# Performance work log

Hardware: AMD Instinct MI355X
Metric: run time of the kernel (lower is better)

## Reference

```python
import jax, jax.numpy as jnp
import numpy as np

B, N, K, D = 16, 16384, 16, 256  # batch, num feature tokens, num slots, slot/feature dim
FEAT = 256
LN_EPS = 1e-5


def _ln(x, g, b):
    m = jnp.mean(x, -1, keepdims=True)
    v = jnp.mean((x - m) ** 2, -1, keepdims=True)
    return (x - m) * jax.lax.rsqrt(v + LN_EPS) * g + b


def setup_inputs() -> dict:
    key = jax.random.key(0)
    ks = jax.random.split(key, 18)
    s = 0.02
    return {
        "features": jax.random.normal(ks[0], (B, N, FEAT), jnp.float32),
        "slots_init": jax.random.normal(ks[1], (B, K, D), jnp.float32),
        "g_f": jnp.ones((FEAT,), jnp.float32), "b_f": jnp.zeros((FEAT,), jnp.float32),
        "g_s": jnp.ones((D,), jnp.float32), "b_s": jnp.zeros((D,), jnp.float32),
        "g_m": jnp.ones((D,), jnp.float32), "b_m": jnp.zeros((D,), jnp.float32),
        "Wq": jax.random.normal(ks[2], (D, D), jnp.float32) * s,
        "Wk": jax.random.normal(ks[3], (D, FEAT), jnp.float32) * s,
        "Wv": jax.random.normal(ks[4], (D, FEAT), jnp.float32) * s,
        "w_ih": jax.random.normal(ks[5], (3 * D, D), jnp.float32) * s,
        "w_hh": jax.random.normal(ks[6], (3 * D, D), jnp.float32) * s,
        "b_ih": jnp.zeros((3 * D,), jnp.float32),
        "b_hh": jnp.zeros((3 * D,), jnp.float32),
        "W1": jax.random.normal(ks[7], (4 * D, D), jnp.float32) * s,
        "b1": jnp.zeros((4 * D,), jnp.float32),
        "W2": jax.random.normal(ks[8], (D, 4 * D), jnp.float32) * s,
        "b2": jnp.zeros((D,), jnp.float32),
        "num_src_view": 4,
    }


def reference(features, slots_init, g_f, b_f, g_s, b_s, g_m, b_m, Wq, Wk, Wv,
              w_ih, w_hh, b_ih, b_hh, W1, b1, W2, b2, num_src_view):
    f = _ln(features, g_f, b_f)            # [B,N,FEAT]
    k = f @ Wk.T                            # [B,N,D]
    v = f @ Wv.T                            # [B,N,D]
    scale = float(D) ** -0.5                # num_head = 1, head-mean is identity

    def gru(x, h):  # PyTorch GRUCell math, batched over [B,K]
        gi = x @ w_ih.T + b_ih
        gh = h @ w_hh.T + b_hh
        ir, iz, inn = jnp.split(gi, 3, -1)
        hr, hz, hn = jnp.split(gh, 3, -1)
        r = jax.nn.sigmoid(ir + hr)
        z = jax.nn.sigmoid(iz + hz)
        n = jnp.tanh(inn + r * hn)
        return (1.0 - z) * n + z * h

    def one_iter(slots):
        q = _ln(slots, g_s, b_s) @ Wq.T                         # [B,K,D]
        logits = jnp.einsum('bkd,bnd->bkn', q, k) * scale       # [B,K,N]
        attn = jax.nn.softmax(logits, axis=1)                   # competitive over slots
        attn_wm = attn / (jnp.sum(attn, -1, keepdims=True) + 1.0)  # epsilon = 1.0
        updates = jnp.einsum('bkn,bnd->bkd', attn_wm, v)        # [B,K,D]
        h = gru(updates, slots)
        h = h + (jax.nn.relu(_ln(h, g_m, b_m) @ W1.T + b1) @ W2.T + b2)
        return h, attn

    slots = slots_init
    for _ in range(2):  # num_iter - 1 iterations with straight-through detach trick
        slots, _ = one_iter(slots)
        slots = jax.lax.stop_gradient(slots) + slots_init - jax.lax.stop_gradient(slots_init)
    slots, attn = one_iter(slots)
    return slots, attn
```

## Files before the change

kernel.cpp:

```cpp
#include <hip/hip_runtime.h>
#include <cstdint>
#include <cstddef>

#define BB    16
#define NTOK  16384
#define KS    16
#define DD    256
#define FEATN 256
#define NBLK  32
#define LN_EPS 1e-5f

typedef float        float4v __attribute__((ext_vector_type(4)));
typedef unsigned int uint4v  __attribute__((ext_vector_type(4)));
typedef unsigned int uint2v  __attribute__((ext_vector_type(2)));
typedef __bf16       bf16x8  __attribute__((ext_vector_type(8)));

__device__ __forceinline__ float bflo(unsigned u){ return __builtin_bit_cast(float, u << 16); }
__device__ __forceinline__ float bfhi(unsigned u){ return __builtin_bit_cast(float, u & 0xffff0000u); }
__device__ __forceinline__ unsigned short f2bf(float v){ __bf16 b = (__bf16)v; return __builtin_bit_cast(unsigned short, b); }
__device__ __forceinline__ float sigm(float x){ return 1.f/(1.f + __expf(-x)); }

__global__ void prep_w_kernel(const float* __restrict__ Wv, const float* __restrict__ w_ih,
                              const float* __restrict__ w_hh, const float* __restrict__ W1,
                              const float* __restrict__ W2, const float* __restrict__ Wq,
                              const float* __restrict__ Wk,
                              unsigned short* __restrict__ Wv_t, unsigned short* __restrict__ wih_t,
                              unsigned short* __restrict__ whh_t, unsigned short* __restrict__ W1_t,
                              unsigned short* __restrict__ W2_t, unsigned short* __restrict__ Wq_t,
                              unsigned short* __restrict__ Wk_b)
{
  __shared__ float tile[64][65];
  const int t = blockIdx.x, tid = threadIdx.x;
  const float* src; unsigned short* dst; int R, C, base;
  if      (t < 16)  { src = Wv;   dst = Wv_t;  R = 256;  C = 256;  base = 0;   }
  else if (t < 64)  { src = w_ih; dst = wih_t; R = 768;  C = 256;  base = 16;  }
  else if (t < 112) { src = w_hh; dst = whh_t; R = 768;  C = 256;  base = 64;  }
  else if (t < 176) { src = W1;   dst = W1_t;  R = 1024; C = 256;  base = 112; }
  else if (t < 240) { src = W2;   dst = W2_t;  R = 256;  C = 1024; base = 176; }
  else if (t < 256) { src = Wq;   dst = Wq_t;  R = 256;  C = 256;  base = 240; }
  else {
    const int t2 = t - 256;
    for (int i = tid; i < 4096; i += 256) {
      const int idx = t2*4096 + i;
      Wk_b[idx] = f2bf(Wk[idx]);
    }
    return;
  }
  const int tt = t - base;
  const int tiles_r = R >> 6;
  const int r0 = (tt % tiles_r) * 64, c0 = (tt / tiles_r) * 64;
  const int j = tid & 63, i0 = (tid >> 6) * 16;
  for (int s = 0; s < 16; ++s)
    tile[i0 + s][j] = src[(size_t)(r0 + i0 + s)*C + c0 + j];
  __syncthreads();
  for (int s = 0; s < 16; ++s) {
    const int i = i0 + s;
    dst[(size_t)(c0 + i)*R + r0 + j] = f2bf(tile[j][i]);
  }
}

__device__ __forceinline__ void lnqu_tail_p(
    const float* Vs, float* Ys, float* Qs, float* Pp, float* SUb, float* CBb,
    const float* __restrict__ g_s, const float* __restrict__ b_s,
    const unsigned short* __restrict__ Wq_t, const unsigned short* __restrict__ Wk_b,
    const float* __restrict__ g_f, const float* __restrict__ b_f,
    unsigned short* __restrict__ u_buf, float* __restrict__ su_buf, float* __restrict__ cb_buf,
    int b, int k0, int tid)
{
  const int w = tid >> 6, L = tid & 63;
  {
    const float v0 = Vs[w*256+L], v1 = Vs[w*256+64+L], v2 = Vs[w*256+128+L], v3 = Vs[w*256+192+L];
    float s = v0+v1+v2+v3;
    #pragma unroll
    for (int m = 1; m < 64; m <<= 1) s += __shfl_xor(s, m);
    const float mean = s * (1.f/DD);
    const float d0 = v0-mean, d1 = v1-mean, d2 = v2-mean, d3 = v3-mean;
    float s2 = d0*d0 + d1*d1 + d2*d2 + d3*d3;
    #pragma unroll
    for (int m = 1; m < 64; m <<= 1) s2 += __shfl_xor(s2, m);
    const float rs = rsqrtf(s2 * (1.f/DD) + LN_EPS);
    Ys[L*4+w]       = d0*rs*g_s[L]      + b_s[L];
    Ys[(64+L)*4+w]  = d1*rs*g_s[64+L]   + b_s[64+L];
    Ys[(128+L)*4+w] = d2*rs*g_s[128+L]  + b_s[128+L];
    Ys[(192+L)*4+w] = d3*rs*g_s[192+L]  + b_s[192+L];
  }
  __syncthreads();
  {
    float acc[4][4] = {};
    for (int cc = w*64; cc < w*64+64; ++cc) {
      const float4v xv = *reinterpret_cast<const float4v*>(Ys + cc*4);
      const uint2v wr = *reinterpret_cast<const uint2v*>(Wq_t + (size_t)cc*DD + 4*L);
      const float w0 = bflo(wr[0]), w1 = bfhi(wr[0]), w2 = bflo(wr[1]), w3 = bfhi(wr[1]);
      #pragma unroll
      for (int s = 0; s < 4; ++s) {
        acc[s][0] += xv[s]*w0; acc[s][1] += xv[s]*w1;
        acc[s][2] += xv[s]*w2; acc[s][3] += xv[s]*w3;
      }
    }
    #pragma unroll
    for (int s = 0; s < 4; ++s)
      *reinterpret_cast<float4v*>(Pp + (w*4+s)*256 + 4*L) = *reinterpret_cast<const float4v*>(acc[s]);
  }
  __syncthreads();
  for (int i = tid; i < 4*DD; i += 256) {
    const int kk = i >> 8, d = i & 255;
    Qs[d*4+kk] = Pp[(0*4+kk)*256+d] + Pp[(1*4+kk)*256+d] + Pp[(2*4+kk)*256+d] + Pp[(3*4+kk)*256+d];
  }
  __syncthreads();
  {
    float acc[4][4] = {};
    for (int d = w*64; d < w*64+64; ++d) {
      const float4v xv = *reinterpret_cast<const float4v*>(Qs + d*4);
      const uint2v wr = *reinterpret_cast<const uint2v*>(Wk_b + (size_t)d*DD + 4*L);
      const float w0 = bflo(wr[0]), w1 = bfhi(wr[0]), w2 = bflo(wr[1]), w3 = bfhi(wr[1]);
      #pragma unroll
      for (int s = 0; s < 4; ++s) {
        acc[s][0] += xv[s]*w0; acc[s][1] += xv[s]*w1;
        acc[s][2] += xv[s]*w2; acc[s][3] += xv[s]*w3;
      }
    }
    #pragma unroll
    for (int s = 0; s < 4; ++s)
      *reinterpret_cast<float4v*>(Pp + (w*4+s)*256 + 4*L) = *reinterpret_cast<const float4v*>(acc[s]);
  }
  __syncthreads();
  for (int i = tid; i < 4*DD; i += 256) {
    const int kk = i >> 8, cc = i & 255;
    const float qk = Pp[(0*4+kk)*256+cc] + Pp[(1*4+kk)*256+cc] + Pp[(2*4+kk)*256+cc] + Pp[(3*4+kk)*256+cc];
    const float uv = qk * g_f[cc];
    u_buf[(size_t)(b*KS + k0 + kk)*DD + cc] = f2bf(uv);
    SUb[kk*256+cc] = uv;
    CBb[kk*256+cc] = qk * b_f[cc];
  }
  __syncthreads();
  {
    float s  = SUb[w*256+L] + SUb[w*256+64+L] + SUb[w*256+128+L] + SUb[w*256+192+L];
    float cv = CBb[w*256+L] + CBb[w*256+64+L] + CBb[w*256+128+L] + CBb[w*256+192+L];
    #pragma unroll
    for (int m = 1; m < 64; m <<= 1) { s += __shfl_xor(s, m); cv += __shfl_xor(cv, m); }
    if (L == 0) { su_buf[b*KS + k0 + w] = s; cb_buf[b*KS + k0 + w] = cv; }
  }
}

__global__ void k0_kernel(const float* __restrict__ slots_init,
                          const float* __restrict__ g_s, const float* __restrict__ b_s,
                          const unsigned short* __restrict__ Wq_t, const unsigned short* __restrict__ Wk_b,
                          const float* __restrict__ g_f, const float* __restrict__ b_f,
                          unsigned short* __restrict__ u_buf, float* __restrict__ su_buf,
                          float* __restrict__ cb_buf)
{
  const int b = blockIdx.x >> 2, k0 = (blockIdx.x & 3) * 4;
  const int tid = threadIdx.x;
  __shared__ __align__(16) float Vs[4*DD];
  __shared__ __align__(16) float Ys[DD*4];
  __shared__ __align__(16) float Qs[DD*4];
  __shared__ __align__(16) float Pp[4*4*DD];
  __shared__ __align__(16) float SUb[4*DD];
  __shared__ __align__(16) float CBb[4*DD];
  for (int i = tid; i < 4*DD; i += 256)
    Vs[i] = slots_init[(size_t)(b*KS + k0)*DD + i];
  __syncthreads();
  lnqu_tail_p(Vs, Ys, Qs, Pp, SUb, CBb, g_s, b_s, Wq_t, Wk_b, g_f, b_f,
              u_buf, su_buf, cb_buf, b, k0, tid);
}

template<int MODE, int LAST>
__launch_bounds__(256, 1)
__global__ void phaseA_kernel(const float* __restrict__ feat,
                              unsigned short* __restrict__ xb, float* __restrict__ stats,
                              const unsigned short* __restrict__ u_buf,
                              const float* __restrict__ su_buf,
                              const float* __restrict__ cb_buf,
                              float* __restrict__ P_part,
                              float* __restrict__ S_part,
                              float* __restrict__ R_part,
                              float* __restrict__ attn_out)
{
  __shared__ __align__(16) unsigned int xl[4][128*36];
  __shared__ float ssh[4][16];
  __shared__ float rsh[4][16];

  const int b   = blockIdx.x / NBLK;
  const int blk = blockIdx.x - b*NBLK;
  const int tid = threadIdx.x;
  const int w = tid >> 6;
  const int l = tid & 63;
  const int c = l & 15;
  const int g = l >> 4;

  bf16x8 ufrag[8];
  {
    const bf16x8* up = reinterpret_cast<const bf16x8*>(u_buf + (size_t)(b*KS + c)*DD);
    #pragma unroll
    for (int kk = 0; kk < 8; ++kk) ufrag[kk] = up[4*kk + g];
  }
  const float su_c = su_buf[b*KS + c];
  const float cb_c = cb_buf[b*KS + c];

  float4v Pacc[16];
  #pragma unroll
  for (int t = 0; t < 16; ++t) Pacc[t] = (float4v){0.f,0.f,0.f,0.f};
  float S_acc = 0.f, R_acc = 0.f;

  unsigned int* myxl = xl[w];
  const int rbase = 8*(c>>2) + (c&3);

  for (int pass = 0; pass < 4; ++pass) {
    const int n0 = blk*(NTOK/NBLK) + pass*128 + w*32;
    float4v Ct[2];
    float m_t[2], rs_t[2];

    if constexpr (MODE == 1) {
      bf16x8 xr0[8], xr1[8];
      float2 st0, st1;
      {
        const size_t row0 = (size_t)b*NTOK + (size_t)(n0 + rbase);
        const size_t row1 = row0 + 4;
        const bf16x8* p0v = reinterpret_cast<const bf16x8*>(xb + row0*FEATN);
        const bf16x8* p1v = reinterpret_cast<const bf16x8*>(xb + row1*FEATN);
        #pragma unroll
        for (int kk = 0; kk < 8; ++kk) { xr0[kk] = p0v[4*kk + g]; xr1[kk] = p1v[4*kk + g]; }
        st0 = *reinterpret_cast<const float2*>(stats + row0*2);
        st1 = *reinterpret_cast<const float2*>(stats + row1*2);
      }
      #pragma unroll
      for (int tp = 0; tp < 2; ++tp) {
        const int nloc = rbase + 4*tp;
        float4v Cacc = (float4v){0.f,0.f,0.f,0.f};
        #pragma unroll
        for (int kk = 0; kk < 8; ++kk) {
          const bf16x8 af = tp ? xr1[kk] : xr0[kk];
          const uint4v ad = __builtin_bit_cast(uint4v, af);
          const int pb = (16*kk + 4*g)*36 + nloc;
          myxl[pb      ] = ad[0];
          myxl[pb + 36 ] = ad[1];
          myxl[pb + 72 ] = ad[2];
          myxl[pb + 108] = ad[3];
          Cacc = __builtin_amdgcn_mfma_f32_16x16x32_bf16(af, ufrag[kk], Cacc, 0, 0, 0);
        }
        m_t[tp]  = tp ? st1.x : st0.x;
        rs_t[tp] = tp ? st1.y : st0.y;
        Ct[tp]   = Cacc;
      }
    } else {
      #pragma unroll
      for (int tp = 0; tp < 2; ++tp) {
        const int nloc = rbase + 4*tp;
        const size_t row = (size_t)b*NTOK + (size_t)(n0 + nloc);
        const float* fr = feat + row*FEATN;
        float4v xf[16];
        #pragma unroll
        for (int kk = 0; kk < 8; ++kk) {
          xf[2*kk]   = *reinterpret_cast<const float4v*>(fr + 32*kk + 8*g);
          xf[2*kk+1] = *reinterpret_cast<const float4v*>(fr + 32*kk + 8*g + 4);
        }
        unsigned short* xw = xb + row*FEATN;
        float sum = 0.f, sq = 0.f;
        float4v Cacc = (float4v){0.f,0.f,0.f,0.f};
        #pragma unroll
        for (int kk = 0; kk < 8; ++kk) {
          const float4v x0 = xf[2*kk], x1 = xf[2*kk+1];
          sum += x0[0]+x0[1]+x0[2]+x0[3] + x1[0]+x1[1]+x1[2]+x1[3];
          sq  += x0[0]*x0[0]+x0[1]*x0[1]+x0[2]*x0[2]+x0[3]*x0[3]
               + x1[0]*x1[0]+x1[1]*x1[1]+x1[2]*x1[2]+x1[3]*x1[3];
          bf16x8 af;
          af[0]=(__bf16)x0[0]; af[1]=(__bf16)x0[1]; af[2]=(__bf16)x0[2]; af[3]=(__bf16)x0[3];
          af[4]=(__bf16)x1[0]; af[5]=(__bf16)x1[1]; af[6]=(__bf16)x1[2]; af[7]=(__bf16)x1[3];
          *reinterpret_cast<bf16x8*>(xw + 32*kk + 8*g) = af;
          const uint4v ad = __builtin_bit_cast(uint4v, af);
          const int pb = (16*kk + 4*g)*36 + nloc;
          myxl[pb      ] = ad[0];
          myxl[pb + 36 ] = ad[1];
          myxl[pb + 72 ] = ad[2];
          myxl[pb + 108] = ad[3];
          Cacc = __builtin_amdgcn_mfma_f32_16x16x32_bf16(af, ufrag[kk], Cacc, 0, 0, 0);
        }
        sum += __shfl_xor(sum,16); sum += __shfl_xor(sum,32);
        sq  += __shfl_xor(sq ,16); sq  += __shfl_xor(sq ,32);
        const float mean = sum * (1.f/FEATN);
        const float var  = sq  * (1.f/FEATN) - mean*mean;
        m_t[tp]  = mean;
        rs_t[tp] = rsqrtf(var + LN_EPS);
        float2 st; st.x = m_t[tp]; st.y = rs_t[tp];
        *reinterpret_cast<float2*>(stats + row*2) = st;
        Ct[tp] = Cacc;
      }
    }

    float arr[8];
    #pragma unroll
    for (int tp = 0; tp < 2; ++tp) {
      float lv[4], rsr[4], mr[4];
      #pragma unroll
      for (int r = 0; r < 4; ++r) {
        const int src = 4*g + r;
        rsr[r] = __shfl(rs_t[tp], src);
        mr[r]  = __shfl(m_t[tp],  src);
        lv[r]  = 0.0625f * (rsr[r]*(Ct[tp][r] - mr[r]*su_c) + cb_c);
      }
      float a_[4];
      #pragma unroll
      for (int r = 0; r < 4; ++r) {
        float v = lv[r];
        v = fmaxf(v, __shfl_xor(v,1));
        v = fmaxf(v, __shfl_xor(v,2));
        v = fmaxf(v, __shfl_xor(v,4));
        v = fmaxf(v, __shfl_xor(v,8));
        const float e = __expf(lv[r] - v);
        float s = e;
        s += __shfl_xor(s,1);
        s += __shfl_xor(s,2);
        s += __shfl_xor(s,4);
        s += __shfl_xor(s,8);
        const float a = e / s;
        a_[r] = a;
        S_acc += a;
        R_acc += a * rsr[r] * mr[r];
        arr[4*tp + r] = a * rsr[r];
      }
      if (LAST) {
        float4v av = {a_[0], a_[1], a_[2], a_[3]};
        *reinterpret_cast<float4v*>(attn_out + (size_t)(b*KS + c)*NTOK + (size_t)(n0 + 8*g + 4*tp)) = av;
      }
    }
    bf16x8 afrag;
    #pragma unroll
    for (int j = 0; j < 8; ++j) afrag[j] = (__bf16)arr[j];

    #pragma unroll
    for (int t = 0; t < 16; ++t) {
      const unsigned int* rp = &myxl[(t*8 + (c>>1))*36 + 8*g];
      const uint4v q0 = *reinterpret_cast<const uint4v*>(rp);
      const uint4v q1 = *reinterpret_cast<const uint4v*>(rp + 4);
      const unsigned int sel = (c & 1) ? 0x07060302u : 0x05040100u;
      uint4v bd;
      bd[0] = __builtin_amdgcn_perm(q0[1], q0[0], sel);
      bd[1] = __builtin_amdgcn_perm(q0[3], q0[2], sel);
      bd[2] = __builtin_amdgcn_perm(q1[1], q1[0], sel);
      bd[3] = __builtin_amdgcn_perm(q1[3], q1[2], sel);
      const bf16x8 bfrag = __builtin_bit_cast(bf16x8, bd);
      Pacc[t] = __builtin_amdgcn_mfma_f32_16x16x32_bf16(afrag, bfrag, Pacc[t], 0, 0, 0);
    }
  }

  S_acc += __shfl_xor(S_acc,16); S_acc += __shfl_xor(S_acc,32);
  R_acc += __shfl_xor(R_acc,16); R_acc += __shfl_xor(R_acc,32);
  if (g == 0) { ssh[w][c] = S_acc; rsh[w][c] = R_acc; }

  float* pf = reinterpret_cast<float*>(myxl);
  #pragma unroll
  for (int t = 0; t < 16; ++t) {
    #pragma unroll
    for (int r = 0; r < 4; ++r) pf[(4*g + r)*256 + t*16 + c] = Pacc[t][r];
  }
  __syncthreads();
  {
    float* outp = P_part + (size_t)blockIdx.x * (KS*DD);
    const float* p0 = reinterpret_cast<const float*>(&xl[0][0]);
    const float* p1 = p0 + 4608;
    const float* p2 = p0 + 9216;
    const float* p3 = p0 + 13824;
    for (int i = tid; i < KS*DD; i += 256) outp[i] = p0[i]+p1[i]+p2[i]+p3[i];
    if (tid < KS) {
      S_part[blockIdx.x*KS + tid] = ssh[0][tid]+ssh[1][tid]+ssh[2][tid]+ssh[3][tid];
      R_part[blockIdx.x*KS + tid] = rsh[0][tid]+rsh[1][tid]+rsh[2][tid]+rsh[3][tid];
    }
  }
}

template<int LAST, int NEXT>
__global__ void fusedB_kernel(const float* __restrict__ P_part, const float* __restrict__ S_part,
                              const float* __restrict__ R_part, const float* __restrict__ slots_in,
                              const float* __restrict__ g_f, const float* __restrict__ b_f,
                              const unsigned short* __restrict__ Wv_t,
                              const unsigned short* __restrict__ wih_t,
                              const unsigned short* __restrict__ whh_t,
                              const float* __restrict__ b_ih, const float* __restrict__ b_hh,
                              const float* __restrict__ g_m, const float* __restrict__ b_m,
                              const unsigned short* __restrict__ W1_t, const float* __restrict__ b1,
                              const unsigned short* __restrict__ W2_t, const float* __restrict__ b2v,
                              const float* __restrict__ g_s, const float* __restrict__ b_s,
                              const unsigned short* __restrict__ Wq_t,
                              const unsigned short* __restrict__ Wk_b,
                              float* __restrict__ slots_next, float* __restrict__ out_slots,
                              unsigned short* __restrict__ u_buf, float* __restrict__ su_buf,
                              float* __restrict__ cb_buf)
{
  const int b = blockIdx.x >> 4, k = blockIdx.x & 15;
  const int tid = threadIdx.x;
  const int w = tid >> 6, L = tid & 63;

  __shared__ __align__(16) float arena[9984];
  __shared__ float SRsh[2];
  __shared__ float redsh[8];

  float* Pp    = arena;
  float* Hsh   = arena + 6144;
  float* Tsh   = arena + 6400;
  float* Ush   = arena + 6656;
  float* Gish  = arena + 6912;
  float* Ghsh  = arena + 7680;
  float* Hpsh  = arena + 8448;
  float* Ysh   = arena + 8704;
  float* Hidsh = arena + 8960;

  Hsh[tid] = slots_in[(size_t)(b*KS + k)*DD + tid];
  if (tid < 64) {
    const int p = tid & 31;
    const float* sp = (tid < 32) ? S_part : R_part;
    float v = sp[(b*NBLK + p)*KS + k];
    v += __shfl_xor(v, 1); v += __shfl_xor(v, 2); v += __shfl_xor(v, 4);
    v += __shfl_xor(v, 8); v += __shfl_xor(v, 16);
    if (p == 0) SRsh[tid >> 5] = v;
  }
  __syncthreads();

  {
    const float S = SRsh[0], R = SRsh[1];
    const float inv = 1.f / (S + 1.f);
    const float* pb = P_part + (size_t)(b*NBLK)*KS*DD + (size_t)k*DD + tid;
    float p0 = 0.f, p1 = 0.f, p2 = 0.f, p3 = 0.f;
    #pragma unroll 2
    for (int p = 0; p < NBLK; p += 4) {
      p0 += pb[(size_t)(p+0)*KS*DD];
      p1 += pb[(size_t)(p+1)*KS*DD];
      p2 += pb[(size_t)(p+2)*KS*DD];
      p3 += pb[(size_t)(p+3)*KS*DD];
    }
    const float P = (p0 + p1) + (p2 + p3);
    Tsh[tid] = (g_f[tid]*(P - R) + S*b_f[tid]) * inv;
  }
  __syncthreads();

  {
    const int c0 = 4*L;
    float a0 = 0.f, a1 = 0.f, a2 = 0.f, a3 = 0.f;
    for (int cc = w*64; cc < w*64+64; ++cc) {
      const float x = Tsh[cc];
      const uint2v wr = *reinterpret_cast<const uint2v*>(Wv_t + (size_t)cc*DD + c0);
      a0 += x*bflo(wr[0]); a1 += x*bfhi(wr[0]);
      a2 += x*bflo(wr[1]); a3 += x*bfhi(wr[1]);
    }
    float4v av = {a0, a1, a2, a3};
    *reinterpret_cast<float4v*>(Pp + w*256 + c0) = av;
  }
  __syncthreads();
  Ush[tid] = Pp[tid] + Pp[256+tid] + Pp[512+tid] + Pp[768+tid];
  __syncthreads();

  {
    const int c0 = 4*L;
    float ai[3][4] = {}, ah[3][4] = {};
    for (int cc = w*64; cc < w*64+64; ++cc) {
      const float xi = Ush[cc], xh = Hsh[cc];
      #pragma unroll
      for (int c = 0; c < 3; ++c) {
        const uint2v wi = *reinterpret_cast<const uint2v*>(wih_t + (size_t)cc*768 + c0 + 256*c);
        const uint2v wh = *reinterpret_cast<const uint2v*>(whh_t + (size_t)cc*768 + c0 + 256*c);
        ai[c][0] += xi*bflo(wi[0]); ai[c][1] += xi*bfhi(wi[0]);
        ai[c][2] += xi*bflo(wi[1]); ai[c][3] += xi*bfhi(wi[1]);
        ah[c][0] += xh*bflo(wh[0]); ah[c][1] += xh*bfhi(wh[0]);
        ah[c][2] += xh*bflo(wh[1]); ah[c][3] += xh*bfhi(wh[1]);
      }
    }
    #pragma unroll
    for (int c = 0; c < 3; ++c) {
      *reinterpret_cast<float4v*>(Pp + w*768 + 256*c + c0)        = *reinterpret_cast<const float4v*>(ai[c]);
      *reinterpret_cast<float4v*>(Pp + 3072 + w*768 + 256*c + c0) = *reinterpret_cast<const float4v*>(ah[c]);
    }
  }
  __syncthreads();
  for (int j = tid; j < 768; j += 256) {
    Gish[j] = b_ih[j] + Pp[j] + Pp[768+j] + Pp[1536+j] + Pp[2304+j];
    Ghsh[j] = b_hh[j] + Pp[3072+j] + Pp[3840+j] + Pp[4608+j] + Pp[5376+j];
  }
  __syncthreads();

  {
    const int d = tid;
    const float r = sigm(Gish[d] + Ghsh[d]);
    const float z = sigm(Gish[256+d] + Ghsh[256+d]);
    const float n = tanhf(Gish[512+d] + r*Ghsh[512+d]);
    const float hp = (1.f - z)*n + z*Hsh[d];
    Hpsh[d] = hp;
    float s = hp;
    #pragma unroll
    for (int m = 1; m < 64; m <<= 1) s += __shfl_xor(s, m);
    if (L == 0) redsh[w] = s;
    __syncthreads();
    const float mean = (redsh[0]+redsh[1]+redsh[2]+redsh[3]) * (1.f/DD);
    const float dv = hp - mean;
    float s2 = dv*dv;
    #pragma unroll
    for (int m = 1; m < 64; m <<= 1) s2 += __shfl_xor(s2, m);
    if (L == 0) redsh[4+w] = s2;
    __syncthreads();
    const float var = (redsh[4]+redsh[5]+redsh[6]+redsh[7]) * (1.f/DD);
    Ysh[d] = dv * rsqrtf(var + LN_EPS) * g_m[d] + b_m[d];
  }
  __syncthreads();

  {
    const int c0 = 4*L;
    float a[4][4] = {};
    for (int cc = w*64; cc < w*64+64; ++cc) {
      const float x = Ysh[cc];
      #pragma unroll
      for (int c = 0; c < 4; ++c) {
        const uint2v wr = *reinterpret_cast<const uint2v*>(W1_t + (size_t)cc*1024 + c0 + 256*c);
        a[c][0] += x*bflo(wr[0]); a[c][1] += x*bfhi(wr[0]);
        a[c][2] += x*bflo(wr[1]); a[c][3] += x*bfhi(wr[1]);
      }
    }
    #pragma unroll
    for (int c = 0; c < 4; ++c)
      *reinterpret_cast<float4v*>(Pp + w*1024 + 256*c + c0) = *reinterpret_cast<const float4v*>(a[c]);
  }
  __syncthreads();
  for (int j = tid; j < 1024; j += 256)
    Hidsh[j] = fmaxf(b1[j] + Pp[j] + Pp[1024+j] + Pp[2048+j] + Pp[3072+j], 0.f);
  __syncthreads();

  {
    const int c0 = 4*L;
    float a0 = 0.f, a1 = 0.f, a2 = 0.f, a3 = 0.f;
    for (int cc = w*256; cc < w*256+256; ++cc) {
      const float x = Hidsh[cc];
      const uint2v wr = *reinterpret_cast<const uint2v*>(W2_t + (size_t)cc*DD + c0);
      a0 += x*bflo(wr[0]); a1 += x*bfhi(wr[0]);
      a2 += x*bflo(wr[1]); a3 += x*bfhi(wr[1]);
    }
    float4v av = {a0, a1, a2, a3};
    *reinterpret_cast<float4v*>(Pp + w*256 + c0) = av;
  }
  __syncthreads();
  {
    const int d = tid;
    const float v = b2v[d] + Pp[d] + Pp[256+d] + Pp[512+d] + Pp[768+d] + Hpsh[d];
    Tsh[d] = v;
    slots_next[(size_t)(b*KS + k)*DD + d] = v;
    if (LAST) out_slots[(size_t)(b*KS + k)*DD + d] = v;
  }

  if constexpr (NEXT) {
    __syncthreads();
    {
      const float v = Tsh[tid];
      float s = v;
      #pragma unroll
      for (int m = 1; m < 64; m <<= 1) s += __shfl_xor(s, m);
      if (L == 0) redsh[w] = s;
      __syncthreads();
      const float mean = (redsh[0]+redsh[1]+redsh[2]+redsh[3]) * (1.f/DD);
      const float dv = v - mean;
      float s2 = dv*dv;
      #pragma unroll
      for (int m = 1; m < 64; m <<= 1) s2 += __shfl_xor(s2, m);
      if (L == 0) redsh[4+w] = s2;
      __syncthreads();
      const float var = (redsh[4]+redsh[5]+redsh[6]+redsh[7]) * (1.f/DD);
      Ush[tid] = dv * rsqrtf(var + LN_EPS) * g_s[tid] + b_s[tid];
    }
    __syncthreads();
    {
      const int c0 = 4*L;
      float a0 = 0.f, a1 = 0.f, a2 = 0.f, a3 = 0.f;
      for (int cc = w*64; cc < w*64+64; ++cc) {
        const float x = Ush[cc];
        const uint2v wr = *reinterpret_cast<const uint2v*>(Wq_t + (size_t)cc*DD + c0);
        a0 += x*bflo(wr[0]); a1 += x*bfhi(wr[0]);
        a2 += x*bflo(wr[1]); a3 += x*bfhi(wr[1]);
      }
      float4v av = {a0, a1, a2, a3};
      *reinterpret_cast<float4v*>(Pp + w*256 + c0) = av;
    }
    __syncthreads();
    Hsh[tid] = Pp[tid] + Pp[256+tid] + Pp[512+tid] + Pp[768+tid];
    __syncthreads();
    {
      const int c0 = 4*L;
      float a0 = 0.f, a1 = 0.f, a2 = 0.f, a3 = 0.f;
      for (int dd = w*64; dd < w*64+64; ++dd) {
        const float x = Hsh[dd];
        const uint2v wr = *reinterpret_cast<const uint2v*>(Wk_b + (size_t)dd*DD + c0);
        a0 += x*bflo(wr[0]); a1 += x*bfhi(wr[0]);
        a2 += x*bflo(wr[1]); a3 += x*bfhi(wr[1]);
      }
      float4v av = {a0, a1, a2, a3};
      *reinterpret_cast<float4v*>(Pp + w*256 + c0) = av;
    }
    __syncthreads();
    {
      const int cidx = tid;
      const float qk = Pp[cidx] + Pp[256+cidx] + Pp[512+cidx] + Pp[768+cidx];
      const float uv = qk * g_f[cidx];
      u_buf[(size_t)(b*KS + k)*DD + cidx] = f2bf(uv);
      float s  = uv;
      float cv = qk * b_f[cidx];
      #pragma unroll
      for (int m = 1; m < 64; m <<= 1) { s += __shfl_xor(s, m); cv += __shfl_xor(cv, m); }
      if (L == 0) { redsh[w] = s; redsh[4+w] = cv; }
      __syncthreads();
      if (tid == 0) {
        su_buf[b*KS + k] = redsh[0]+redsh[1]+redsh[2]+redsh[3];
        cb_buf[b*KS + k] = redsh[4]+redsh[5]+redsh[6]+redsh[7];
      }
    }
  }
}

extern "C" void kernel_launch(void* const* d_in, const int* in_sizes, int n_in,
                              void* d_out, int out_size, void* d_ws, size_t ws_size,
                              hipStream_t stream)
{
  const float* features   = (const float*)d_in[0];
  const float* slots_init = (const float*)d_in[1];
  const float* g_f = (const float*)d_in[2];
  const float* b_f = (const float*)d_in[3];
  const float* g_s = (const float*)d_in[4];
  const float* b_s = (const float*)d_in[5];
  const float* g_m = (const float*)d_in[6];
  const float* b_m = (const float*)d_in[7];
  const float* Wq  = (const float*)d_in[8];
  const float* Wk  = (const float*)d_in[9];
  const float* Wv  = (const float*)d_in[10];
  const float* w_ih = (const float*)d_in[11];
  const float* w_hh = (const float*)d_in[12];
  const float* b_ih = (const float*)d_in[13];
  const float* b_hh = (const float*)d_in[14];
  const float* W1  = (const float*)d_in[15];
  const float* b1  = (const float*)d_in[16];
  const float* W2  = (const float*)d_in[17];
  const float* b2  = (const float*)d_in[18];

  float* out_slots = (float*)d_out;
  float* out_attn  = out_slots + (size_t)BB*KS*DD;

  char* ws = (char*)d_ws;
  size_t off = 0;
  auto alloc = [&](size_t bytes) -> void* {
    void* p = ws + off;
    off += (bytes + 255) & ~(size_t)255;
    return p;
  };
  unsigned short* u_buf  = (unsigned short*)alloc((size_t)BB*KS*DD*2);
  float*          su_buf = (float*)alloc((size_t)BB*KS*4);
  float*          cb_buf = (float*)alloc((size_t)BB*KS*4);
  float*          P_part = (float*)alloc((size_t)BB*NBLK*KS*DD*4);
  float*          S_part = (float*)alloc((size_t)BB*NBLK*KS*4);
  float*          R_part = (float*)alloc((size_t)BB*NBLK*KS*4);
  float*          slots_ws = (float*)alloc((size_t)BB*KS*DD*4);
  unsigned short* Wv_t  = (unsigned short*)alloc((size_t)256*256*2);
  unsigned short* wih_t = (unsigned short*)alloc((size_t)256*768*2);
  unsigned short* whh_t = (unsigned short*)alloc((size_t)256*768*2);
  unsigned short* W1_t  = (unsigned short*)alloc((size_t)256*1024*2);
  unsigned short* W2_t  = (unsigned short*)alloc((size_t)1024*256*2);
  unsigned short* Wq_t  = (unsigned short*)alloc((size_t)256*256*2);
  unsigned short* Wk_b  = (unsigned short*)alloc((size_t)256*256*2);
  float*          stats = (float*)alloc((size_t)BB*NTOK*2*4);
  unsigned short* xb    = (unsigned short*)alloc((size_t)BB*NTOK*FEATN*2);
  (void)in_sizes; (void)n_in; (void)out_size; (void)ws_size;

  prep_w_kernel<<<272, 256, 0, stream>>>(Wv, w_ih, w_hh, W1, W2, Wq, Wk,
                                         Wv_t, wih_t, whh_t, W1_t, W2_t, Wq_t, Wk_b);
  k0_kernel<<<BB*4, 256, 0, stream>>>(slots_init, g_s, b_s, Wq_t, Wk_b, g_f, b_f,
                                      u_buf, su_buf, cb_buf);

  phaseA_kernel<0,0><<<BB*NBLK, 256, 0, stream>>>(features, xb, stats, u_buf, su_buf, cb_buf,
                                                  P_part, S_part, R_part, out_attn);
  fusedB_kernel<0,1><<<BB*KS, 256, 0, stream>>>(P_part, S_part, R_part, slots_init, g_f, b_f,
                                                Wv_t, wih_t, whh_t, b_ih, b_hh, g_m, b_m,
                                                W1_t, b1, W2_t, b2, g_s, b_s, Wq_t, Wk_b,
                                                slots_ws, out_slots, u_buf, su_buf, cb_buf);
  phaseA_kernel<1,0><<<BB*NBLK, 256, 0, stream>>>(features, xb, stats, u_buf, su_buf, cb_buf,
                                                  P_part, S_part, R_part, out_attn);
  fusedB_kernel<0,1><<<BB*KS, 256, 0, stream>>>(P_part, S_part, R_part, slots_ws, g_f, b_f,
                                                Wv_t, wih_t, whh_t, b_ih, b_hh, g_m, b_m,
                                                W1_t, b1, W2_t, b2, g_s, b_s, Wq_t, Wk_b,
                                                slots_ws, out_slots, u_buf, su_buf, cb_buf);
  phaseA_kernel<1,1><<<BB*NBLK, 256, 0, stream>>>(features, xb, stats, u_buf, su_buf, cb_buf,
                                                  P_part, S_part, R_part, out_attn);
  fusedB_kernel<1,0><<<BB*KS, 256, 0, stream>>>(P_part, S_part, R_part, slots_ws, g_f, b_f,
                                                Wv_t, wih_t, whh_t, b_ih, b_hh, g_m, b_m,
                                                W1_t, b1, W2_t, b2, g_s, b_s, Wq_t, Wk_b,
                                                slots_ws, out_slots, u_buf, su_buf, cb_buf);
}
```

Measured before the change: 401.4 us.

## Halve phaseA shared-memory tile for MODE 1 and raise occupancy hints

For the MODE 1 (bf16 reuse) phase-A kernel, the shared transpose tile is halved by staging the feature tile into LDS in two 128-column halves, each followed by its P-accumulation MFMAs. The partial-P reduction is likewise done in two halves. Launch bounds now request 2 or 4 blocks per CU so more waves can be resident to hide memory latency. The risks are register pressure from the raised occupancy hint and extra barriers in the epilogue.

```diff
diff --git a/kernel.cpp b/kernel.cpp
--- a/kernel.cpp
+++ b/kernel.cpp
@@ -165,7 +165,7 @@
 }
 
 template<int MODE, int LAST>
-__launch_bounds__(256, 1)
+__launch_bounds__(256, (MODE==0) ? 2 : 4)
 __global__ void phaseA_kernel(const float* __restrict__ feat,
                               unsigned short* __restrict__ xb, float* __restrict__ stats,
                               const unsigned short* __restrict__ u_buf,
@@ -176,7 +176,8 @@
                               float* __restrict__ R_part,
                               float* __restrict__ attn_out)
 {
-  __shared__ __align__(16) unsigned int xl[4][128*36];
+  constexpr int TP = (MODE==0) ? 128*36 : 64*36;
+  __shared__ __align__(16) unsigned int xl[4][TP];
   __shared__ float ssh[4][16];
   __shared__ float rsh[4][16];
 
@@ -225,22 +226,87 @@
       }
       #pragma unroll
       for (int tp = 0; tp < 2; ++tp) {
-        const int nloc = rbase + 4*tp;
         float4v Cacc = (float4v){0.f,0.f,0.f,0.f};
         #pragma unroll
         for (int kk = 0; kk < 8; ++kk) {
           const bf16x8 af = tp ? xr1[kk] : xr0[kk];
-          const uint4v ad = __builtin_bit_cast(uint4v, af);
-          const int pb = (16*kk + 4*g)*36 + nloc;
-          myxl[pb      ] = ad[0];
-          myxl[pb + 36 ] = ad[1];
-          myxl[pb + 72 ] = ad[2];
-          myxl[pb + 108] = ad[3];
           Cacc = __builtin_amdgcn_mfma_f32_16x16x32_bf16(af, ufrag[kk], Cacc, 0, 0, 0);
         }
         m_t[tp]  = tp ? st1.x : st0.x;
         rs_t[tp] = tp ? st1.y : st0.y;
         Ct[tp]   = Cacc;
+      }
+      float arr[8];
+      #pragma unroll
+      for (int tp = 0; tp < 2; ++tp) {
+        float lv[4], rsr[4], mr[4];
+        #pragma unroll
+        for (int r = 0; r < 4; ++r) {
+          const int src = 4*g + r;
+          rsr[r] = __shfl(rs_t[tp], src);
+          mr[r]  = __shfl(m_t[tp],  src);
+          lv[r]  = 0.0625f * (rsr[r]*(Ct[tp][r] - mr[r]*su_c) + cb_c);
+        }
+        float a_[4];
+        #pragma unroll
+        for (int r = 0; r < 4; ++r) {
+          float v = lv[r];
+          v = fmaxf(v, __shfl_xor(v,1));
+          v = fmaxf(v, __shfl_xor(v,2));
+          v = fmaxf(v, __shfl_xor(v,4));
+          v = fmaxf(v, __shfl_xor(v,8));
+          const float e = __expf(lv[r] - v);
+          float s = e;
+          s += __shfl_xor(s,1);
+          s += __shfl_xor(s,2);
+          s += __shfl_xor(s,4);
+          s += __shfl_xor(s,8);
+          const float a = e / s;
+          a_[r] = a;
+          S_acc += a;
+          R_acc += a * rsr[r] * mr[r];
+          arr[4*tp + r] = a * rsr[r];
+        }
+        if (LAST) {
+          float4v av = {a_[0], a_[1], a_[2], a_[3]};
+          *reinterpret_cast<float4v*>(attn_out + (size_t)(b*KS + c)*NTOK + (size_t)(n0 + 8*g + 4*tp)) = av;
+        }
+      }
+      bf16x8 afrag;
+      #pragma unroll
+      for (int j = 0; j < 8; ++j) afrag[j] = (__bf16)arr[j];
+
+      #pragma unroll
+      for (int h = 0; h < 2; ++h) {
+        #pragma unroll
+        for (int kk = 4*h; kk < 4*h+4; ++kk) {
+          const uint4v a0 = __builtin_bit_cast(uint4v, xr0[kk]);
+          const uint4v a1 = __builtin_bit_cast(uint4v, xr1[kk]);
+          const int pb = (16*kk + 4*g - 64*h)*36;
+          myxl[pb       + rbase    ] = a0[0];
+          myxl[pb + 36  + rbase    ] = a0[1];
+          myxl[pb + 72  + rbase    ] = a0[2];
+          myxl[pb + 108 + rbase    ] = a0[3];
+          myxl[pb       + rbase + 4] = a1[0];
+          myxl[pb + 36  + rbase + 4] = a1[1];
+          myxl[pb + 72  + rbase + 4] = a1[2];
+          myxl[pb + 108 + rbase + 4] = a1[3];
+        }
+        #pragma unroll
+        for (int t2 = 0; t2 < 8; ++t2) {
+          const int t = 8*h + t2;
+          const unsigned int* rp = &myxl[(t2*8 + (c>>1))*36 + 8*g];
+          const uint4v q0 = *reinterpret_cast<const uint4v*>(rp);
+          const uint4v q1 = *reinterpret_cast<const uint4v*>(rp + 4);
+          const unsigned int sel = (c & 1) ? 0x07060302u : 0x05040100u;
+          uint4v bd;
+          bd[0] = __builtin_amdgcn_perm(q0[1], q0[0], sel);
+          bd[1] = __builtin_amdgcn_perm(q0[3], q0[2], sel);
+          bd[2] = __builtin_amdgcn_perm(q1[1], q1[0], sel);
+          bd[3] = __builtin_amdgcn_perm(q1[3], q1[2], sel);
+          const bf16x8 bfrag = __builtin_bit_cast(bf16x8, bd);
+          Pacc[t] = __builtin_amdgcn_mfma_f32_16x16x32_bf16(afrag, bfrag, Pacc[t], 0, 0, 0);
+        }
       }
     } else {
       #pragma unroll
@@ -285,61 +351,61 @@
         *reinterpret_cast<float2*>(stats + row*2) = st;
         Ct[tp] = Cacc;
       }
-    }
-
-    float arr[8];
-    #pragma unroll
-    for (int tp = 0; tp < 2; ++tp) {
-      float lv[4], rsr[4], mr[4];
-      #pragma unroll
-      for (int r = 0; r < 4; ++r) {
-        const int src = 4*g + r;
-        rsr[r] = __shfl(rs_t[tp], src);
-        mr[r]  = __shfl(m_t[tp],  src);
-        lv[r]  = 0.0625f * (rsr[r]*(Ct[tp][r] - mr[r]*su_c) + cb_c);
-      }
-      float a_[4];
-      #pragma unroll
-      for (int r = 0; r < 4; ++r) {
-        float v = lv[r];
-        v = fmaxf(v, __shfl_xor(v,1));
-        v = fmaxf(v, __shfl_xor(v,2));
-        v = fmaxf(v, __shfl_xor(v,4));
-        v = fmaxf(v, __shfl_xor(v,8));
-        const float e = __expf(lv[r] - v);
-        float s = e;
-        s += __shfl_xor(s,1);
-        s += __shfl_xor(s,2);
-        s += __shfl_xor(s,4);
-        s += __shfl_xor(s,8);
-        const float a = e / s;
-        a_[r] = a;
-        S_acc += a;
-        R_acc += a * rsr[r] * mr[r];
-        arr[4*tp + r] = a * rsr[r];
-      }
-      if (LAST) {
-        float4v av = {a_[0], a_[1], a_[2], a_[3]};
-        *reinterpret_cast<float4v*>(attn_out + (size_t)(b*KS + c)*NTOK + (size_t)(n0 + 8*g + 4*tp)) = av;
-      }
-    }
-    bf16x8 afrag;
-    #pragma unroll
-    for (int j = 0; j < 8; ++j) afrag[j] = (__bf16)arr[j];
-
-    #pragma unroll
-    for (int t = 0; t < 16; ++t) {
-      const unsigned int* rp = &myxl[(t*8 + (c>>1))*36 + 8*g];
-      const uint4v q0 = *reinterpret_cast<const uint4v*>(rp);
-      const uint4v q1 = *reinterpret_cast<const uint4v*>(rp + 4);
-      const unsigned int sel = (c & 1) ? 0x07060302u : 0x05040100u;
-      uint4v bd;
-      bd[0] = __builtin_amdgcn_perm(q0[1], q0[0], sel);
-      bd[1] = __builtin_amdgcn_perm(q0[3], q0[2], sel);
-      bd[2] = __builtin_amdgcn_perm(q1[1], q1[0], sel);
-      bd[3] = __builtin_amdgcn_perm(q1[3], q1[2], sel);
-      const bf16x8 bfrag = __builtin_bit_cast(bf16x8, bd);
-      Pacc[t] = __builtin_amdgcn_mfma_f32_16x16x32_bf16(afrag, bfrag, Pacc[t], 0, 0, 0);
+
+      float arr[8];
+      #pragma unroll
+      for (int tp = 0; tp < 2; ++tp) {
+        float lv[4], rsr[4], mr[4];
+        #pragma unroll
+        for (int r = 0; r < 4; ++r) {
+          const int src = 4*g + r;
+          rsr[r] = __shfl(rs_t[tp], src);
+          mr[r]  = __shfl(m_t[tp],  src);
+          lv[r]  = 0.0625f * (rsr[r]*(Ct[tp][r] - mr[r]*su_c) + cb_c);
+        }
+        float a_[4];
+        #pragma unroll
+        for (int r = 0; r < 4; ++r) {
+          float v = lv[r];
+          v = fmaxf(v, __shfl_xor(v,1));
+          v = fmaxf(v, __shfl_xor(v,2));
+          v = fmaxf(v, __shfl_xor(v,4));
+          v = fmaxf(v, __shfl_xor(v,8));
+          const float e = __expf(lv[r] - v);
+          float s = e;
+          s += __shfl_xor(s,1);
+          s += __shfl_xor(s,2);
+          s += __shfl_xor(s,4);
+          s += __shfl_xor(s,8);
+          const float a = e / s;
+          a_[r] = a;
+          S_acc += a;
+          R_acc += a * rsr[r] * mr[r];
+          arr[4*tp + r] = a * rsr[r];
+        }
+        if (LAST) {
+          float4v av = {a_[0], a_[1], a_[2], a_[3]};
+          *reinterpret_cast<float4v*>(attn_out + (size_t)(b*KS + c)*NTOK + (size_t)(n0 + 8*g + 4*tp)) = av;
+        }
+      }
+      bf16x8 afrag;
+      #pragma unroll
+      for (int j = 0; j < 8; ++j) afrag[j] = (__bf16)arr[j];
+
+      #pragma unroll
+      for (int t = 0; t < 16; ++t) {
+        const unsigned int* rp = &myxl[(t*8 + (c>>1))*36 + 8*g];
+        const uint4v q0 = *reinterpret_cast<const uint4v*>(rp);
+        const uint4v q1 = *reinterpret_cast<const uint4v*>(rp + 4);
+        const unsigned int sel = (c & 1) ? 0x07060302u : 0x05040100u;
+        uint4v bd;
+        bd[0] = __builtin_amdgcn_perm(q0[1], q0[0], sel);
+        bd[1] = __builtin_amdgcn_perm(q0[3], q0[2], sel);
+        bd[2] = __builtin_amdgcn_perm(q1[1], q1[0], sel);
+        bd[3] = __builtin_amdgcn_perm(q1[3], q1[2], sel);
+        const bf16x8 bfrag = __builtin_bit_cast(bf16x8, bd);
+        Pacc[t] = __builtin_amdgcn_mfma_f32_16x16x32_bf16(afrag, bfrag, Pacc[t], 0, 0, 0);
+      }
     }
   }
 
@@ -347,20 +413,48 @@
   R_acc += __shfl_xor(R_acc,16); R_acc += __shfl_xor(R_acc,32);
   if (g == 0) { ssh[w][c] = S_acc; rsh[w][c] = R_acc; }
 
-  float* pf = reinterpret_cast<float*>(myxl);
-  #pragma unroll
-  for (int t = 0; t < 16; ++t) {
-    #pragma unroll
-    for (int r = 0; r < 4; ++r) pf[(4*g + r)*256 + t*16 + c] = Pacc[t][r];
-  }
-  __syncthreads();
-  {
-    float* outp = P_part + (size_t)blockIdx.x * (KS*DD);
-    const float* p0 = reinterpret_cast<const float*>(&xl[0][0]);
-    const float* p1 = p0 + 4608;
-    const float* p2 = p0 + 9216;
-    const float* p3 = p0 + 13824;
-    for (int i = tid; i < KS*DD; i += 256) outp[i] = p0[i]+p1[i]+p2[i]+p3[i];
+  if constexpr (MODE == 0) {
+    float* pf = reinterpret_cast<float*>(myxl);
+    #pragma unroll
+    for (int t = 0; t < 16; ++t) {
+      #pragma unroll
+      for (int r = 0; r < 4; ++r) pf[(4*g + r)*256 + t*16 + c] = Pacc[t][r];
+    }
+    __syncthreads();
+    {
+      float* outp = P_part + (size_t)blockIdx.x * (KS*DD);
+      const float* p0 = reinterpret_cast<const float*>(&xl[0][0]);
+      const float* p1 = p0 + TP;
+      const float* p2 = p0 + 2*TP;
+      const float* p3 = p0 + 3*TP;
+      for (int i = tid; i < KS*DD; i += 256) outp[i] = p0[i]+p1[i]+p2[i]+p3[i];
+      if (tid < KS) {
+        S_part[blockIdx.x*KS + tid] = ssh[0][tid]+ssh[1][tid]+ssh[2][tid]+ssh[3][tid];
+        R_part[blockIdx.x*KS + tid] = rsh[0][tid]+rsh[1][tid]+rsh[2][tid]+rsh[3][tid];
+      }
+    }
+  } else {
+    float* pf = reinterpret_cast<float*>(myxl);
+    #pragma unroll
+    for (int half = 0; half < 2; ++half) {
+      __syncthreads();
+      #pragma unroll
+      for (int t2 = 0; t2 < 8; ++t2) {
+        #pragma unroll
+        for (int r = 0; r < 4; ++r)
+          pf[(4*g + r)*128 + t2*16 + c] = Pacc[half*8 + t2][r];
+      }
+      __syncthreads();
+      float* outp = P_part + (size_t)blockIdx.x * (KS*DD) + half*128;
+      const float* p0 = reinterpret_cast<const float*>(&xl[0][0]);
+      const float* p1 = p0 + TP;
+      const float* p2 = p0 + 2*TP;
+      const float* p3 = p0 + 3*TP;
+      for (int i = tid; i < 2048; i += 256) {
+        const int rowk = i >> 7, rem = i & 127;
+        outp[rowk*256 + rem] = p0[i] + p1[i] + p2[i] + p3[i];
+      }
+    }
     if (tid < KS) {
       S_part[blockIdx.x*KS + tid] = ssh[0][tid]+ssh[1][tid]+ssh[2][tid]+ssh[3][tid];
       R_part[blockIdx.x*KS + tid] = rsh[0][tid]+rsh[1][tid]+rsh[2][tid]+rsh[3][tid];
```

Result: slower. 502.1 us (+25.1%).
